# Performance work log

Measured on AMD Instinct MI355X. Metric: run time of the kernel, lower is better.

## Reference

```python
import jax, jax.numpy as jnp
import numpy as np

B, C_IN, H, W = 4096, 3, 32, 32
C1, C2, K = 32, 64, 3
FC1, NCLS = 256, 10


def _extract_patches(x):
    # x: (B, C, H, W) -> patches (B, C, K*K, H, W), 3x3 neighborhoods, pad=1
    xp = jnp.pad(x, ((0, 0), (0, 0), (1, 1), (1, 1)))
    shifts = [xp[:, :, i:i + H, j:j + W] for i in range(K) for j in range(K)]
    return jnp.stack(shifts, axis=2)


def _maxpool2(x):
    b, c, h, w = x.shape
    return x.reshape(b, c, h // 2, 2, w // 2, 2).max(axis=(3, 5))


def setup_inputs() -> dict:
    key = jax.random.key(0)
    ks = jax.random.split(key, 9)
    # kaiming-ish scales
    s_lc = np.sqrt(2.0 / (C_IN * K * K)).astype(np.float32)
    s_cv = np.sqrt(2.0 / (C1 * K * K)).astype(np.float32)
    s_f1 = np.sqrt(2.0 / (C2 * 8 * 8)).astype(np.float32)
    s_f2 = np.sqrt(2.0 / FC1).astype(np.float32)
    return {
        "x": jax.random.normal(ks[0], (B, C_IN, H, W), dtype=jnp.float32),
        # unshared per-location weights: (O, C, K*K, H, W)
        "w_lc": jax.random.normal(ks[1], (C1, C_IN, K * K, H, W), dtype=jnp.float32) * s_lc,
        "b_lc": jnp.zeros((C1, H, W), dtype=jnp.float32),
        "w_conv": jax.random.normal(ks[2], (C2, C1, K, K), dtype=jnp.float32) * s_cv,
        "b_conv": jnp.zeros((C2,), dtype=jnp.float32),
        "w_fc1": jax.random.normal(ks[3], (FC1, C2 * 8 * 8), dtype=jnp.float32) * s_f1,
        "b_fc1": jnp.zeros((FC1,), dtype=jnp.float32),
        "w_fc2": jax.random.normal(ks[4], (NCLS, FC1), dtype=jnp.float32) * s_f2,
        "b_fc2": jnp.zeros((NCLS,), dtype=jnp.float32),
    }


def reference(x, w_lc, b_lc, w_conv, b_conv, w_fc1, b_fc1, w_fc2, b_fc2):
    # locally connected layer: per-(i,j) unshared 3x3 filters
    patches = _extract_patches(x)                                  # (B, C, 9, H, W)
    y = jnp.einsum('bckij,ockij->boij', patches, w_lc) + b_lc[None]  # (B, C1, H, W)
    y = jax.nn.relu(y)
    y = _maxpool2(y)                                               # (B, C1, 16, 16)
    # standard 3x3 conv, padding SAME
    y = jax.lax.conv_general_dilated(
        y, w_conv, window_strides=(1, 1), padding='SAME',
        dimension_numbers=('NCHW', 'OIHW', 'NCHW'))
    y = jax.nn.relu(y + b_conv[None, :, None, None])
    y = _maxpool2(y)                                               # (B, C2, 8, 8)
    y = y.reshape(y.shape[0], -1)                                  # (B, C2*8*8)
    y = jax.nn.relu(y @ w_fc1.T + b_fc1)
    return y @ w_fc2.T + b_fc2                                     # (B, num_classes)
```

## Files before the change

kernel.cpp:

```cpp
#include <hip/hip_runtime.h>

typedef short s16x8 __attribute__((ext_vector_type(8)));
typedef float f32x4 __attribute__((ext_vector_type(4)));
typedef unsigned short u16x4 __attribute__((ext_vector_type(4)));

static __device__ __forceinline__ unsigned short f2bf(float f) {
    union { float f; unsigned u; } v; v.f = f;
    unsigned r = v.u + 0x7FFF + ((v.u >> 16) & 1);
    return (unsigned short)(r >> 16);
}

__global__ __launch_bounds__(256) void k_prep(
    const float* __restrict__ w_lc, const float* __restrict__ b_lc,
    const float* __restrict__ w_conv, const float* __restrict__ w_fc1,
    unsigned short* __restrict__ wpk, unsigned short* __restrict__ wt_g,
    unsigned short* __restrict__ Wb)
{
    const int t = threadIdx.x, bx = blockIdx.x;
    if (bx < 64) {
        __shared__ unsigned short wtile[16 * 1024];
        const int p0 = bx * 16;
        for (int f = t; f < 8192; f += 256) ((int*)wtile)[f] = 0;
        __syncthreads();
        for (int f = t; f < 13824; f += 256) {
            const int row = f >> 4, pl = f & 15;
            const int o = row / 27, ck = row - o * 27;
            wtile[(pl * 32 + o) * 32 + ck] = f2bf(w_lc[(size_t)row * 1024 + p0 + pl]);
        }
        for (int f = t; f < 512; f += 256) {
            const int o = f >> 4, pl = f & 15;
            wtile[(pl * 32 + o) * 32 + 27] = f2bf(b_lc[o * 1024 + p0 + pl]);
        }
        __syncthreads();
        const int4* s = (const int4*)wtile;
        int4* d = (int4*)(wpk + (size_t)p0 * 1024);
        for (int f = t; f < 2048; f += 256) d[f] = s[f];
    } else if (bx < 128) {
        const float4* wf4 = (const float4*)w_fc1;
        for (int f = t; f < 4096; f += 256) {
            const int idx = (bx - 64) * 4096 + f;
            const float4 v = wf4[idx];
            u16x4 o = { f2bf(v.x), f2bf(v.y), f2bf(v.z), f2bf(v.w) };
            *(u16x4*)&Wb[idx * 4] = o;
        }
    } else {
        for (int i = t; i < 9 * 64 * 40; i += 256) wt_g[i] = 0;
        __syncthreads();
        for (int i = t; i < 64 * 32 * 9; i += 256) {
            const int oc = i / 288;
            const int rem = i - oc * 288;
            const int ic = rem / 9;
            const int kk = rem - ic * 9;
            wt_g[(kk * 64 + oc) * 40 + ic] = f2bf(w_conv[i]);
        }
    }
}

__global__ __launch_bounds__(256, 5) void k_lc(
    const float* __restrict__ x,
    const unsigned short* __restrict__ wpk,
    unsigned short* __restrict__ y1g)
{
    __shared__ unsigned short xb[12 * 34 * 17];
    __shared__ unsigned short pbuf[8][16][40];
    const int t = threadIdx.x;
    const int ib = blockIdx.x >> 4;
    const int pr = blockIdx.x & 15;
    const int img0 = ib * 16;

    for (int f = t; f < 3468; f += 256) ((int*)xb)[f] = 0;
    __syncthreads();
    for (int f = t; f < 6144; f += 256) {
        const int img = f / 384;
        const int rem = f - img * 384;
        const int c = rem >> 7;
        const int rr = (rem >> 5) & 3;
        const int col = rem & 31;
        const int xrow = 2 * pr - 1 + rr;
        if ((unsigned)xrow < 32u) {
            const float v = x[((size_t)(img0 + img) * 3 + c) * 1024 + xrow * 32 + col];
            xb[((c * 4 + rr) * 34 + col + 1) * 17 + img] = f2bf(v);
        }
    }
    __syncthreads();

    const int lane = t & 63, wv = t >> 6;
    const int lc = lane & 15, lg = lane >> 4;
    const int parity = wv & 1, nfh = wv >> 1;
    const int o = nfh * 16 + lc;

    int abase[8];
    #pragma unroll
    for (int e = 0; e < 8; ++e) {
        int k = lg * 8 + e; if (k > 26) k = 26;
        const int c = k / 9, dd = k - c * 9, di = dd / 3, dj = dd - di * 3;
        abase[e] = ((c * 4 + di) * 34 + dj) * 17 + lc;
    }

    for (int ph = 0; ph < 2; ++ph) {
        for (int jj = 0; jj < 4; ++jj) {
            const int jp = ph * 8 + jj * 2 + parity;
            s16x8 bfr[4];
            #pragma unroll
            for (int pos = 0; pos < 4; ++pos) {
                const int ih = pos >> 1, jc = pos & 1;
                const int p = (2 * pr + ih) * 32 + jp * 2 + jc;
                bfr[pos] = *(const s16x8*)&wpk[((size_t)p * 32 + o) * 32 + lg * 8];
            }
            f32x4 acc4[4];
            #pragma unroll
            for (int pos = 0; pos < 4; ++pos) {
                const int ih = pos >> 1, jc = pos & 1;
                const int off = ih * 578 + (jp * 2 + jc) * 17;
                int r[8];
                #pragma unroll
                for (int e = 0; e < 8; ++e) r[e] = xb[abase[e] + off];
                if (lg == 3) r[3] = 0x3F80;
                int4 ai = { r[0] | (r[1] << 16), r[2] | (r[3] << 16),
                            r[4] | (r[5] << 16), r[6] | (r[7] << 16) };
                const s16x8 a = __builtin_bit_cast(s16x8, ai);
                f32x4 z = {0.f, 0.f, 0.f, 0.f};
                acc4[pos] = __builtin_amdgcn_mfma_f32_16x16x32_bf16(a, bfr[pos], z, 0, 0, 0);
            }
            #pragma unroll
            for (int q = 0; q < 4; ++q) {
                const float m = fmaxf(fmaxf(fmaxf(acc4[0][q], acc4[1][q]),
                                            fmaxf(acc4[2][q], acc4[3][q])), 0.f);
                pbuf[jp & 7][lg * 4 + q][o] = f2bf(m);
            }
        }
        __syncthreads();
        for (int c = t; c < 512; c += 256) {
            const int img = c >> 5;
            const int rem = c & 31;
            const int jph = rem >> 2;
            const int u = rem & 3;
            *(s16x8*)&y1g[((((size_t)(img0 + img) * 16 + pr) * 16
                            + ph * 8 + jph) * 32) + u * 8] =
                *(const s16x8*)&pbuf[jph][img][u * 8];
        }
        __syncthreads();
    }
}

__global__ __launch_bounds__(256, 2) void k_conv(
    const unsigned short* __restrict__ y1g,
    const unsigned short* __restrict__ wt_g,
    const float* __restrict__ b_conv,
    unsigned short* __restrict__ p2)
{
    __shared__ __align__(16) unsigned short y1t[18][18][40];
    __shared__ __align__(16) unsigned short wt[9 * 64 * 40];
    __shared__ __align__(16) unsigned short pbuf[4][1024];
    const int t = threadIdx.x;
    const int img = blockIdx.x;

    {
        const s16x8 z = {0, 0, 0, 0, 0, 0, 0, 0};
        unsigned short* p = &y1t[0][0][0];
        for (int i = t * 8; i < 18 * 18 * 40; i += 2048) *(s16x8*)(p + i) = z;
        const s16x8* src = (const s16x8*)wt_g;
        s16x8* dst = (s16x8*)wt;
        for (int i = t; i < (9 * 64 * 40) / 8; i += 256) dst[i] = src[i];
    }
    __syncthreads();
    {
        const int prr = t >> 4, pcc = t & 15;
        const unsigned short* src = y1g + ((size_t)img * 256 + t) * 32;
        unsigned short* d = &y1t[prr + 1][pcc + 1][0];
        #pragma unroll
        for (int ch = 0; ch < 4; ++ch)
            *(s16x8*)(d + ch * 8) = *(const s16x8*)(src + ch * 8);
    }
    __syncthreads();

    const int w = t >> 6, lane = t & 63;
    const int lc = lane & 15, lg = lane >> 4;

    f32x4 acc[4][4];
    #pragma unroll
    for (int mf = 0; mf < 4; ++mf)
        #pragma unroll
        for (int nf = 0; nf < 4; ++nf) {
            f32x4 zz = {0.f, 0.f, 0.f, 0.f};
            acc[mf][nf] = zz;
        }
    #pragma unroll
    for (int kk = 0; kk < 9; ++kk) {
        const int di = kk / 3, dj = kk % 3;
        s16x8 a[4], bb[4];
        #pragma unroll
        for (int mf = 0; mf < 4; ++mf)
            a[mf] = *(const s16x8*)&y1t[w * 4 + mf + di][lc + dj][lg * 8];
        #pragma unroll
        for (int nf = 0; nf < 4; ++nf)
            bb[nf] = *(const s16x8*)&wt[(kk * 64 + nf * 16 + lc) * 40 + lg * 8];
        #pragma unroll
        for (int mf = 0; mf < 4; ++mf)
            #pragma unroll
            for (int nf = 0; nf < 4; ++nf)
                acc[mf][nf] = __builtin_amdgcn_mfma_f32_16x16x32_bf16(
                    a[mf], bb[nf], acc[mf][nf], 0, 0, 0);
    }
    #pragma unroll
    for (int mfp = 0; mfp < 2; ++mfp) {
        #pragma unroll
        for (int nf = 0; nf < 4; ++nf) {
            const f32x4 u = acc[mfp * 2][nf], v = acc[mfp * 2 + 1][nf];
            const float bbv = b_conv[nf * 16 + lc];
            float q0 = fmaxf(fmaxf(u[0], u[1]), fmaxf(v[0], v[1]));
            float q1 = fmaxf(fmaxf(u[2], u[3]), fmaxf(v[2], v[3]));
            q0 = fmaxf(q0 + bbv, 0.f);
            q1 = fmaxf(q1 + bbv, 0.f);
            *(unsigned*)&pbuf[w][(nf * 16 + lc) * 16 + mfp * 8 + lg * 2] =
                (unsigned)f2bf(q0) | ((unsigned)f2bf(q1) << 16);
        }
    }
    #pragma unroll
    for (int jj = 0; jj < 2; ++jj) {
        const int u8 = jj * 64 + lane;
        const int oc = u8 >> 1, s = (u8 & 1) * 8;
        const s16x8 val = *(const s16x8*)&pbuf[w][u8 * 8];
        *(s16x8*)&p2[((size_t)img * 64 + oc) * 64 + w * 16 + s] = val;
    }
}

__global__ __launch_bounds__(256) void k_fc1(
    const unsigned short* __restrict__ A,
    const unsigned short* __restrict__ Wb,
    const float* __restrict__ bias, float* __restrict__ out)
{
    __shared__ __align__(16) unsigned short As[64][72];
    __shared__ __align__(16) unsigned short Bs[32][72];
    const int t = threadIdx.x;
    const int m0 = blockIdx.x * 64, n0 = blockIdx.y * 32;
    const int w = t >> 6, lane = t & 63;
    const int lc = lane & 15, lg = lane >> 4;
    f32x4 acc[2];
    {
        f32x4 z = {0.f, 0.f, 0.f, 0.f};
        acc[0] = z; acc[1] = z;
    }
    for (int k0 = 0; k0 < 4096; k0 += 64) {
        {
            const int r0 = t >> 3, ch0 = (t & 7) * 8;
            const int id1 = t + 256;
            const int r1 = id1 >> 3, ch1 = (id1 & 7) * 8;
            *(s16x8*)&As[r0][ch0] = *(const s16x8*)&A[(size_t)(m0 + r0) * 4096 + k0 + ch0];
            *(s16x8*)&As[r1][ch1] = *(const s16x8*)&A[(size_t)(m0 + r1) * 4096 + k0 + ch1];
            const int rb = t >> 3, cb = (t & 7) * 8;
            *(s16x8*)&Bs[rb][cb] = *(const s16x8*)&Wb[(size_t)(n0 + rb) * 4096 + k0 + cb];
        }
        __syncthreads();
        #pragma unroll
        for (int kh = 0; kh < 2; ++kh) {
            const s16x8 a  = *(const s16x8*)&As[w * 16 + lc][kh * 32 + lg * 8];
            const s16x8 b0 = *(const s16x8*)&Bs[lc][kh * 32 + lg * 8];
            const s16x8 b1 = *(const s16x8*)&Bs[16 + lc][kh * 32 + lg * 8];
            acc[0] = __builtin_amdgcn_mfma_f32_16x16x32_bf16(a, b0, acc[0], 0, 0, 0);
            acc[1] = __builtin_amdgcn_mfma_f32_16x16x32_bf16(a, b1, acc[1], 0, 0, 0);
        }
        __syncthreads();
    }
    #pragma unroll
    for (int nf = 0; nf < 2; ++nf) {
        const int n = n0 + nf * 16 + lc;
        const float bv = bias[n];
        #pragma unroll
        for (int q = 0; q < 4; ++q) {
            const int m = m0 + w * 16 + lg * 4 + q;
            out[(size_t)m * 256 + n] = fmaxf(acc[nf][q] + bv, 0.f);
        }
    }
}

__global__ __launch_bounds__(320) void k_fc2(
    const float* __restrict__ fc1, const float* __restrict__ Wt,
    const float* __restrict__ bias, float* __restrict__ out)
{
    const int t = threadIdx.x;
    const int r = blockIdx.x * 32 + t / 10;
    const int n = t % 10;
    const float4* a = (const float4*)(fc1 + (size_t)r * 256);
    const float4* w = (const float4*)(Wt + (size_t)n * 256);
    float acc = bias[n];
    #pragma unroll 8
    for (int k = 0; k < 64; ++k) {
        const float4 av = a[k], wv = w[k];
        acc += av.x * wv.x + av.y * wv.y + av.z * wv.z + av.w * wv.w;
    }
    out[(size_t)r * 10 + n] = acc;
}

extern "C" void kernel_launch(void* const* d_in, const int* in_sizes, int n_in,
                              void* d_out, int out_size, void* d_ws, size_t ws_size,
                              hipStream_t stream)
{
    const float* x      = (const float*)d_in[0];
    const float* w_lc   = (const float*)d_in[1];
    const float* b_lc   = (const float*)d_in[2];
    const float* w_conv = (const float*)d_in[3];
    const float* b_conv = (const float*)d_in[4];
    const float* w_fc1  = (const float*)d_in[5];
    const float* b_fc1  = (const float*)d_in[6];
    const float* w_fc2  = (const float*)d_in[7];
    const float* b_fc2  = (const float*)d_in[8];
    float* out = (float*)d_out;

    unsigned short* p2b  = (unsigned short*)d_ws;
    unsigned short* wpk  = (unsigned short*)((char*)d_ws + 16777216);
    unsigned short* y1g  = (unsigned short*)((char*)d_ws + 33554432);
    float*          fc1  = (float*)((char*)d_ws + 33554432);
    unsigned short* Wb   = (unsigned short*)((char*)d_ws + 67108864);
    unsigned short* wt_g = (unsigned short*)((char*)d_ws + 69206016);

    k_prep<<<129, 256, 0, stream>>>(w_lc, b_lc, w_conv, w_fc1, wpk, wt_g, Wb);
    for (int half = 0; half < 2; ++half) {
        k_lc<<<2048, 256, 0, stream>>>(x + (size_t)half * 2048 * 3072, wpk, y1g);
        k_conv<<<2048, 256, 0, stream>>>(y1g, wt_g, b_conv,
                                         p2b + (size_t)half * 2048 * 4096);
    }
    k_fc1<<<dim3(64, 8), 256, 0, stream>>>(p2b, Wb, b_fc1, fc1);
    k_fc2<<<128, 320, 0, stream>>>(fc1, w_fc2, b_fc2, out);
}
```

Baseline: 199.6 us.

## Restructure locally-connected layer as 4x4 input-window MFMA with folded pooling

Weights for the locally connected layer are repacked so each 2x2 pooling window shares one 4x4 input patch (48 inputs plus a bias slot, K=64). The four output positions of a window and the output channels form the N dimension of the MFMA. Pooling is done with lane shuffles instead of separate accumulators. Each block now handles 32 images with float4 input loads, and the shared-memory layout lets A fragments be built from packed 32-bit loads instead of scalar gathers. In exchange the weight table is larger, the prep kernel does more work, and occupancy drops from 5 to 4 blocks.

```diff
diff --git a/kernel.cpp b/kernel.cpp
--- a/kernel.cpp
+++ b/kernel.cpp
@@ -13,32 +13,43 @@
 __global__ __launch_bounds__(256) void k_prep(
     const float* __restrict__ w_lc, const float* __restrict__ b_lc,
     const float* __restrict__ w_conv, const float* __restrict__ w_fc1,
-    unsigned short* __restrict__ wpk, unsigned short* __restrict__ wt_g,
+    unsigned short* __restrict__ btab, unsigned short* __restrict__ wt_g,
     unsigned short* __restrict__ Wb)
 {
     const int t = threadIdx.x, bx = blockIdx.x;
-    if (bx < 64) {
-        __shared__ unsigned short wtile[16 * 1024];
-        const int p0 = bx * 16;
-        for (int f = t; f < 8192; f += 256) ((int*)wtile)[f] = 0;
-        __syncthreads();
-        for (int f = t; f < 13824; f += 256) {
-            const int row = f >> 4, pl = f & 15;
-            const int o = row / 27, ck = row - o * 27;
-            wtile[(pl * 32 + o) * 32 + ck] = f2bf(w_lc[(size_t)row * 1024 + p0 + pl]);
-        }
-        for (int f = t; f < 512; f += 256) {
-            const int o = f >> 4, pl = f & 15;
-            wtile[(pl * 32 + o) * 32 + 27] = f2bf(b_lc[o * 1024 + p0 + pl]);
-        }
-        __syncthreads();
-        const int4* s = (const int4*)wtile;
-        int4* d = (int4*)(wpk + (size_t)p0 * 1024);
-        for (int f = t; f < 2048; f += 256) d[f] = s[f];
-    } else if (bx < 128) {
+    if (bx < 1024) {
+        const int gid = bx * 256 + t;
+        const int k8 = gid & 7;
+        const int nn = (gid >> 3) & 127;
+        const int jp = (gid >> 10) & 15;
+        const int pr = gid >> 14;
+        const int o = nn >> 2, ih = (nn >> 1) & 1, jc = nn & 1;
+        const int row = 2 * pr + ih, col = 2 * jp + jc;
+        unsigned v32[8];
+        #pragma unroll
+        for (int e = 0; e < 8; ++e) {
+            const int k = k8 * 8 + e;
+            float v = 0.f;
+            if (k < 48) {
+                const int c = k >> 4, rr = (k >> 2) & 3, cf = k & 3;
+                const int di = rr - ih, dj = cf - jc;
+                if ((unsigned)di < 3u && (unsigned)dj < 3u)
+                    v = w_lc[((o * 3 + c) * 9 + di * 3 + dj) * 1024 + row * 32 + col];
+            } else if (k == 63) {
+                v = b_lc[o * 1024 + row * 32 + col];
+            }
+            v32[e] = f2bf(v);
+        }
+        uint4 w;
+        w.x = v32[0] | (v32[1] << 16);
+        w.y = v32[2] | (v32[3] << 16);
+        w.z = v32[4] | (v32[5] << 16);
+        w.w = v32[6] | (v32[7] << 16);
+        *(uint4*)&btab[(size_t)gid * 8] = w;
+    } else if (bx < 1088) {
         const float4* wf4 = (const float4*)w_fc1;
         for (int f = t; f < 4096; f += 256) {
-            const int idx = (bx - 64) * 4096 + f;
+            const int idx = (bx - 1024) * 4096 + f;
             const float4 v = wf4[idx];
             u16x4 o = { f2bf(v.x), f2bf(v.y), f2bf(v.z), f2bf(v.w) };
             *(u16x4*)&Wb[idx * 4] = o;
@@ -56,88 +67,131 @@
     }
 }
 
-__global__ __launch_bounds__(256, 5) void k_lc(
+__global__ __launch_bounds__(256, 4) void k_lc(
     const float* __restrict__ x,
-    const unsigned short* __restrict__ wpk,
+    const unsigned short* __restrict__ btab,
     unsigned short* __restrict__ y1g)
 {
-    __shared__ unsigned short xb[12 * 34 * 17];
-    __shared__ unsigned short pbuf[8][16][40];
+    __shared__ unsigned short xb_raw[8 + 12 * 34 * 34 + 8];
+    __shared__ unsigned short pbuf[4][32][40];
     const int t = threadIdx.x;
     const int ib = blockIdx.x >> 4;
     const int pr = blockIdx.x & 15;
-    const int img0 = ib * 16;
-
-    for (int f = t; f < 3468; f += 256) ((int*)xb)[f] = 0;
+    const int img0 = ib * 32;
+    unsigned short* xbp = xb_raw + 8;
+
+    for (int f = t; f < (8 + 12 * 34 * 34 + 8) / 2; f += 256) ((int*)xb_raw)[f] = 0;
     __syncthreads();
-    for (int f = t; f < 6144; f += 256) {
-        const int img = f / 384;
-        const int rem = f - img * 384;
-        const int c = rem >> 7;
-        const int rr = (rem >> 5) & 3;
-        const int col = rem & 31;
+    #pragma unroll
+    for (int i = 0; i < 12; ++i) {
+        const int f = t + i * 256;
+        const int img = f / 96;
+        const int rem = f - img * 96;
+        const int c = rem >> 5, rr = (rem >> 3) & 3, cf = rem & 7;
         const int xrow = 2 * pr - 1 + rr;
         if ((unsigned)xrow < 32u) {
-            const float v = x[((size_t)(img0 + img) * 3 + c) * 1024 + xrow * 32 + col];
-            xb[((c * 4 + rr) * 34 + col + 1) * 17 + img] = f2bf(v);
+            const float4 v = *(const float4*)&x[
+                ((size_t)(img0 + img) * 3 + c) * 1024 + xrow * 32 + cf * 4];
+            const unsigned w0 = (unsigned)f2bf(v.x) | ((unsigned)f2bf(v.y) << 16);
+            const unsigned w1 = (unsigned)f2bf(v.z) | ((unsigned)f2bf(v.w) << 16);
+            const int imgl = (img & 15) + (img >> 4) * 17;
+            const int sa = ((c * 4 + rr) * 34 + imgl) * 34 + cf * 4;
+            *(unsigned*)&xbp[sa] = w0;
+            *(unsigned*)&xbp[sa + 2] = w1;
         }
     }
     __syncthreads();
 
     const int lane = t & 63, wv = t >> 6;
     const int lc = lane & 15, lg = lane >> 4;
-    const int parity = wv & 1, nfh = wv >> 1;
-    const int o = nfh * 16 + lc;
-
-    int abase[8];
-    #pragma unroll
-    for (int e = 0; e < 8; ++e) {
-        int k = lg * 8 + e; if (k > 26) k = 26;
-        const int c = k / 9, dd = k - c * 9, di = dd / 3, dj = dd - di * 3;
-        abase[e] = ((c * 4 + di) * 34 + dj) * 17 + lc;
-    }
-
-    for (int ph = 0; ph < 2; ++ph) {
+
+    for (int g = 0; g < 4; ++g) {
         for (int jj = 0; jj < 4; ++jj) {
-            const int jp = ph * 8 + jj * 2 + parity;
-            s16x8 bfr[4];
+            const int jp = g * 4 + jj;
+            const int colb = jp * 2 - 1;
+            const unsigned short* bp = btab + ((size_t)(pr * 16 + jp) * 128 + wv * 32) * 64;
+            s16x8 B00 = *(const s16x8*)&bp[(lc) * 64 + lg * 8];
+            s16x8 B01 = *(const s16x8*)&bp[(16 + lc) * 64 + lg * 8];
+            s16x8 B10 = *(const s16x8*)&bp[(lc) * 64 + 32 + lg * 8];
+            s16x8 B11 = *(const s16x8*)&bp[(16 + lc) * 64 + 32 + lg * 8];
+
+            f32x4 acc[2][2];
             #pragma unroll
-            for (int pos = 0; pos < 4; ++pos) {
-                const int ih = pos >> 1, jc = pos & 1;
-                const int p = (2 * pr + ih) * 32 + jp * 2 + jc;
-                bfr[pos] = *(const s16x8*)&wpk[((size_t)p * 32 + o) * 32 + lg * 8];
-            }
-            f32x4 acc4[4];
+            for (int mh = 0; mh < 2; ++mh)
+                #pragma unroll
+                for (int nf = 0; nf < 2; ++nf) {
+                    f32x4 z = {0.f, 0.f, 0.f, 0.f};
+                    acc[mh][nf] = z;
+                }
+
             #pragma unroll
-            for (int pos = 0; pos < 4; ++pos) {
-                const int ih = pos >> 1, jc = pos & 1;
-                const int off = ih * 578 + (jp * 2 + jc) * 17;
-                int r[8];
-                #pragma unroll
-                for (int e = 0; e < 8; ++e) r[e] = xb[abase[e] + off];
-                if (lg == 3) r[3] = 0x3F80;
-                int4 ai = { r[0] | (r[1] << 16), r[2] | (r[3] << 16),
-                            r[4] | (r[5] << 16), r[6] | (r[7] << 16) };
-                const s16x8 a = __builtin_bit_cast(s16x8, ai);
-                f32x4 z = {0.f, 0.f, 0.f, 0.f};
-                acc4[pos] = __builtin_amdgcn_mfma_f32_16x16x32_bf16(a, bfr[pos], z, 0, 0, 0);
+            for (int mh = 0; mh < 2; ++mh) {
+                const int mbase = mh * 17 + lc;
+                {
+                    unsigned w[4];
+                    #pragma unroll
+                    for (int rI = 0; rI < 2; ++rI) {
+                        const int base = ((lg * 2 + rI) * 34 + mbase) * 34 + colb - 1;
+                        const unsigned d0 = *(const unsigned*)&xbp[base];
+                        const unsigned d1 = *(const unsigned*)&xbp[base + 2];
+                        const unsigned d2 = *(const unsigned*)&xbp[base + 4];
+                        w[rI * 2 + 0] = (unsigned)(((((unsigned long long)d1) << 32) | d0) >> 16);
+                        w[rI * 2 + 1] = (unsigned)(((((unsigned long long)d2) << 32) | d1) >> 16);
+                    }
+                    uint4 ai = { w[0], w[1], w[2], w[3] };
+                    const s16x8 a = __builtin_bit_cast(s16x8, ai);
+                    acc[mh][0] = __builtin_amdgcn_mfma_f32_16x16x32_bf16(a, B00, acc[mh][0], 0, 0, 0);
+                    acc[mh][1] = __builtin_amdgcn_mfma_f32_16x16x32_bf16(a, B01, acc[mh][1], 0, 0, 0);
+                }
+                {
+                    const int r0 = (8 + lg * 2 > 11) ? 11 : 8 + lg * 2;
+                    const int r1 = (9 + lg * 2 > 11) ? 11 : 9 + lg * 2;
+                    unsigned w[4];
+                    const int rows[2] = { r0, r1 };
+                    #pragma unroll
+                    for (int rI = 0; rI < 2; ++rI) {
+                        const int base = (rows[rI] * 34 + mbase) * 34 + colb - 1;
+                        const unsigned d0 = *(const unsigned*)&xbp[base];
+                        const unsigned d1 = *(const unsigned*)&xbp[base + 2];
+                        const unsigned d2 = *(const unsigned*)&xbp[base + 4];
+                        w[rI * 2 + 0] = (unsigned)(((((unsigned long long)d1) << 32) | d0) >> 16);
+                        w[rI * 2 + 1] = (unsigned)(((((unsigned long long)d2) << 32) | d1) >> 16);
+                    }
+                    w[3] = (lg == 3) ? 0x3F800000u : w[3];
+                    uint4 ai = { w[0], w[1], w[2], w[3] };
+                    const s16x8 a = __builtin_bit_cast(s16x8, ai);
+                    acc[mh][0] = __builtin_amdgcn_mfma_f32_16x16x32_bf16(a, B10, acc[mh][0], 0, 0, 0);
+                    acc[mh][1] = __builtin_amdgcn_mfma_f32_16x16x32_bf16(a, B11, acc[mh][1], 0, 0, 0);
+                }
             }
             #pragma unroll
-            for (int q = 0; q < 4; ++q) {
-                const float m = fmaxf(fmaxf(fmaxf(acc4[0][q], acc4[1][q]),
-                                            fmaxf(acc4[2][q], acc4[3][q])), 0.f);
-                pbuf[jp & 7][lg * 4 + q][o] = f2bf(m);
-            }
-        }
-        __syncthreads();
-        for (int c = t; c < 512; c += 256) {
-            const int img = c >> 5;
-            const int rem = c & 31;
-            const int jph = rem >> 2;
-            const int u = rem & 3;
-            *(s16x8*)&y1g[((((size_t)(img0 + img) * 16 + pr) * 16
-                            + ph * 8 + jph) * 32) + u * 8] =
-                *(const s16x8*)&pbuf[jph][img][u * 8];
+            for (int mh = 0; mh < 2; ++mh)
+                #pragma unroll
+                for (int nf = 0; nf < 2; ++nf) {
+                    f32x4 v = acc[mh][nf];
+                    #pragma unroll
+                    for (int q = 0; q < 4; ++q) {
+                        float a = v[q];
+                        a = fmaxf(a, __shfl_xor(a, 1, 64));
+                        a = fmaxf(a, __shfl_xor(a, 2, 64));
+                        v[q] = a;
+                    }
+                    const float sel = (lc & 2) ? ((lc & 1) ? v[3] : v[2])
+                                               : ((lc & 1) ? v[1] : v[0]);
+                    const float m = fmaxf(sel, 0.f);
+                    pbuf[jp & 3][mh * 16 + lg * 4 + (lc & 3)]
+                        [wv * 8 + nf * 4 + (lc >> 2)] = f2bf(m);
+                }
+        }
+        __syncthreads();
+        {
+            const int img = t >> 3, jpq = (t >> 1) & 3, hf = t & 1;
+            const int jpg = g * 4 + jpq;
+            const s16x8* s = (const s16x8*)&pbuf[jpq][img][hf * 16];
+            s16x8* d = (s16x8*)&y1g[(((size_t)(img0 + img) * 256) + pr * 16 + jpg) * 32
+                                    + hf * 16];
+            d[0] = s[0];
+            d[1] = s[1];
         }
         __syncthreads();
     }
@@ -308,15 +362,15 @@
     float* out = (float*)d_out;
 
     unsigned short* p2b  = (unsigned short*)d_ws;
-    unsigned short* wpk  = (unsigned short*)((char*)d_ws + 16777216);
+    unsigned short* btab = (unsigned short*)((char*)d_ws + 16777216);
     unsigned short* y1g  = (unsigned short*)((char*)d_ws + 33554432);
     float*          fc1  = (float*)((char*)d_ws + 33554432);
     unsigned short* Wb   = (unsigned short*)((char*)d_ws + 67108864);
     unsigned short* wt_g = (unsigned short*)((char*)d_ws + 69206016);
 
-    k_prep<<<129, 256, 0, stream>>>(w_lc, b_lc, w_conv, w_fc1, wpk, wt_g, Wb);
+    k_prep<<<1089, 256, 0, stream>>>(w_lc, b_lc, w_conv, w_fc1, btab, wt_g, Wb);
     for (int half = 0; half < 2; ++half) {
-        k_lc<<<2048, 256, 0, stream>>>(x + (size_t)half * 2048 * 3072, wpk, y1g);
+        k_lc<<<1024, 256, 0, stream>>>(x + (size_t)half * 2048 * 3072, btab, y1g);
         k_conv<<<2048, 256, 0, stream>>>(y1g, wt_g, b_conv,
                                          p2b + (size_t)half * 2048 * 4096);
     }
```

Measured after the change: 222.9 us. 1.12x slower.
